# Kernel optimization log

Hardware: AMD Instinct MI355X
Metric: run time of the kernel (lower is better)

The kernel has to match this reference:

```python
import jax, jax.numpy as jnp
import numpy as np

B, S, D = 2, 4096, 768
H = 12
HD = D // H  # 64


def setup_inputs() -> dict:
    key = jax.random.key(0)
    ks = jax.random.split(key, 5)
    scale = 1.0 / np.sqrt(D)
    x = jax.random.normal(ks[0], (B, S, D), dtype=jnp.float32)
    Wq = jax.random.normal(ks[1], (D, D), dtype=jnp.float32) * scale
    Wk = jax.random.normal(ks[2], (D, D), dtype=jnp.float32) * scale
    Wv = jax.random.normal(ks[3], (D, D), dtype=jnp.float32) * scale
    Wo = jax.random.normal(ks[4], (D, D), dtype=jnp.float32) * scale
    zb = jnp.zeros((D,), dtype=jnp.float32)
    return {"x": x, "Wq": Wq, "bq": zb, "Wk": Wk, "bk": zb, "Wv": Wv, "bv": zb, "Wo": Wo, "bo": zb}


def reference(x, Wq, bq, Wk, bk, Wv, bv, Wo, bo):
    b, s, d = x.shape
    # projections: nn.Linear computes x @ W^T + b; here W is stored as [in, out]-style [D, D]
    def proj(W, bias):
        y = jnp.einsum('bsd,ed->bse', x, W) + bias  # matches torch Linear (weight [out,in])
        return y.reshape(b, s, H, HD).transpose(0, 2, 1, 3)  # [B,H,S,HD]
    q = proj(Wq, bq)
    k = proj(Wk, bk)
    v = proj(Wv, bv)
    att = jnp.einsum('bhqd,bhkd->bhqk', q, k) / np.sqrt(HD).astype(np.float32)
    causal = jnp.tril(jnp.ones((s, s), dtype=bool))
    att = jnp.where(causal, att, -jnp.inf)
    att = jax.nn.softmax(att, axis=-1)  # dropout p=0 (eval)
    y = jnp.einsum('bhqk,bhkd->bhqd', att, v)
    y = y.transpose(0, 2, 1, 3).reshape(b, s, d)
    return jnp.einsum('bsd,ed->bse', y, Wo) + bo
```

## Files before the change

kernel.cpp:

```cpp
#include <hip/hip_runtime.h>
#include <hip/hip_bf16.h>

typedef __bf16 bf16;
typedef __attribute__((ext_vector_type(8))) __bf16 bf16x8;
typedef __attribute__((ext_vector_type(4))) __bf16 bf16x4;
typedef __attribute__((ext_vector_type(4))) float f32x4;
typedef __attribute__((ext_vector_type(16))) float f32x16;

#if __has_builtin(__builtin_amdgcn_permlane32_swap)
#define HAVE_PLSWAP 1
typedef __attribute__((ext_vector_type(2))) unsigned uint2v;
#endif

#define MFMA16(a, b, c) __builtin_amdgcn_mfma_f32_16x16x32_bf16((a), (b), (c), 0, 0, 0)
#define MFMA32(a, b, c) __builtin_amdgcn_mfma_f32_32x32x16_bf16((a), (b), (c), 0, 0, 0)

__device__ __forceinline__ void gload_lds16(const bf16* g, bf16* l) {
  __builtin_amdgcn_global_load_lds(
      (const __attribute__((address_space(1))) void*)g,
      (__attribute__((address_space(3))) void*)l, 16, 0, 0);
}

__device__ __forceinline__ unsigned pkbf(float a, float b) {
  union { unsigned u; bf16 h[2]; } w;
  w.h[0] = (bf16)a; w.h[1] = (bf16)b;
  return w.u;
}

__device__ __forceinline__ float mx3(float a, float b, float c) {
  return fmaxf(fmaxf(a, b), c);
}

__global__ void cvt_all(const float* __restrict__ x,
                        const float* __restrict__ wq, const float* __restrict__ wk,
                        const float* __restrict__ wv, const float* __restrict__ wo,
                        bf16* __restrict__ xb, bf16* __restrict__ Wb) {
  constexpr int NX4 = 6291456 / 4;
  constexpr int NW4 = 589824 / 4;
  constexpr int TOT = NX4 + 4 * NW4;
  int stride = gridDim.x * blockDim.x;
  for (int i = blockIdx.x * blockDim.x + threadIdx.x; i < TOT; i += stride) {
    const float4* src;
    bf16x4* dst;
    if (i < NX4) {
      src = reinterpret_cast<const float4*>(x) + i;
      dst = reinterpret_cast<bf16x4*>(xb) + i;
    } else {
      int j = i - NX4;
      int w = j / NW4, r = j - w * NW4;
      const float* sp = (w == 0) ? wq : (w == 1) ? wk : (w == 2) ? wv : wo;
      src = reinterpret_cast<const float4*>(sp) + r;
      dst = reinterpret_cast<bf16x4*>(Wb) + j;
    }
    float4 v = *src;
    bf16x4 o = {(bf16)v.x, (bf16)v.y, (bf16)v.z, (bf16)v.w};
    *dst = o;
  }
}

template <bool OUT_BF16>
__global__ __launch_bounds__(256) void gemm_bt(
    const bf16* __restrict__ A, const bf16* __restrict__ W,
    const float* __restrict__ b0, const float* __restrict__ b1, const float* __restrict__ b2,
    float* __restrict__ Cf, bf16* __restrict__ Cb,
    int M, int N, int K) {
  const int z = blockIdx.z;
  const bf16* Wz = W + (size_t)z * N * K;
  const float* bias = (z == 0) ? b0 : (z == 1 ? b1 : b2);

  __shared__ alignas(16) bf16 As[128 * 64];
  __shared__ alignas(16) bf16 Bs[128 * 64];

  const int tid = threadIdx.x;
  const int wave = tid >> 6, lane = tid & 63;
  const int lr = lane & 15, lg = lane >> 4;
  const int wr = wave >> 1, wc = wave & 1;
  const int m0 = blockIdx.y * 128, n0 = blockIdx.x * 128;

  f32x4 acc[4][4] = {};

  for (int k0 = 0; k0 < K; k0 += 64) {
    __syncthreads();
#pragma unroll
    for (int j = 0; j < 4; ++j) {
      int cb = j * 256 + wave * 64;
      int c = cb + lane;
      int row = c >> 3, x = c & 7;
      int xs = x ^ (row & 7);
      gload_lds16(&A[(size_t)(m0 + row) * K + k0 + xs * 8], &As[cb * 8]);
      gload_lds16(&Wz[(size_t)(n0 + row) * K + k0 + xs * 8], &Bs[cb * 8]);
    }
    __syncthreads();
#pragma unroll
    for (int kk = 0; kk < 2; ++kk) {
      bf16x8 af[4], bfr[4];
#pragma unroll
      for (int m = 0; m < 4; ++m) {
        int row = wr * 64 + m * 16 + lr;
        int ch = (kk * 4 + lg) ^ (row & 7);
        af[m] = *reinterpret_cast<const bf16x8*>(&As[row * 64 + ch * 8]);
      }
#pragma unroll
      for (int n = 0; n < 4; ++n) {
        int row = wc * 64 + n * 16 + lr;
        int ch = (kk * 4 + lg) ^ (row & 7);
        bfr[n] = *reinterpret_cast<const bf16x8*>(&Bs[row * 64 + ch * 8]);
      }
      __builtin_amdgcn_s_setprio(1);
#pragma unroll
      for (int m = 0; m < 4; ++m)
#pragma unroll
        for (int n = 0; n < 4; ++n)
          acc[m][n] = MFMA16(af[m], bfr[n], acc[m][n]);
      __builtin_amdgcn_s_setprio(0);
    }
  }

#pragma unroll
  for (int m = 0; m < 4; ++m) {
#pragma unroll
    for (int n = 0; n < 4; ++n) {
#pragma unroll
      for (int i = 0; i < 4; ++i) {
        int row = m0 + wr * 64 + m * 16 + lg * 4 + i;
        int col = n0 + wc * 64 + n * 16 + lr;
        float v = acc[m][n][i] + bias[col];
        if constexpr (OUT_BF16)
          (Cb + (size_t)z * M * N)[(size_t)row * N + col] = (bf16)v;
        else
          Cf[(size_t)row * N + col] = v;
      }
    }
  }
}

__global__ __launch_bounds__(256, 3) void attn32(
    const bf16* __restrict__ Q, const bf16* __restrict__ K,
    const bf16* __restrict__ V, bf16* __restrict__ Y) {
  constexpr int S = 4096, D = 768;
  const int lin = blockIdx.x + 32 * blockIdx.y + 384 * blockIdx.z;
  const int xcd = lin & 7, idx = lin >> 3;
  const int pair = xcd * 3 + (idx >> 5);
  const int qb = 31 - (idx & 31);
  const int h = pair % 12, bb = pair / 12;

  const int tid = threadIdx.x, wave = tid >> 6, lane = tid & 63;
  const int ln = lane & 31, hi = lane >> 5;
  const int q0 = qb * 128;
  const int qw0 = q0 + wave * 32;
  const int qrow = qw0 + ln;

  __shared__ alignas(16) bf16 Ks[2][64 * 64];
  __shared__ alignas(16) bf16 Vt[2][64 * 64];

  const size_t head = (size_t)bb * S * D + (size_t)h * 64;
  const float SC2 = 0.125f * 1.44269504089f;

  union U32x4 { unsigned u[4]; bf16x8 v; };
  U32x4 onesU;
  onesU.u[0] = onesU.u[1] = onesU.u[2] = onesU.u[3] = 0x3F803F80u;
  const bf16x8 onesf = onesU.v;

  bf16x8 qf[4];
  {
    const bf16* qp = Q + head + (size_t)qrow * D;
#pragma unroll
    for (int c = 0; c < 4; ++c) {
      bf16x8 t = *reinterpret_cast<const bf16x8*>(qp + c * 16 + hi * 8);
#pragma unroll
      for (int e = 0; e < 8; ++e) t[e] = (bf16)((float)t[e] * SC2);
      qf[c] = t;
    }
  }

  int fOff[4];
#pragma unroll
  for (int i = 0; i < 4; ++i)
    fOff[i] = ln * 64 + ((((2 * i + hi) ^ ln) & 7) * 8);

  const int d0 = (tid >> 5) * 8, k0v = ln * 2;
  int wOff[8];
#pragma unroll
  for (int e = 0; e < 8; ++e)
    wOff[e] = (d0 + e) * 64 + ((((ln >> 2) ^ e) & 7) * 8) + (k0v & 7);

  const bf16* gk[2];
  int ldsK[2];
#pragma unroll
  for (int j = 0; j < 2; ++j) {
    int c = (j * 4 + wave) * 64 + lane;
    int r = c >> 3;
    int src = (((lane ^ r) & 7)) * 8;
    gk[j] = K + head + (size_t)r * D + src;
    ldsK[j] = (j * 4 + wave) * 512;
  }
  const bf16* gv0 = V + head + (size_t)k0v * D + d0;
  const bf16* gv1 = gv0 + D;

  f32x16 accO0 = {}, accO1 = {}, accL = {};
  float mrun = 8.0f;

  auto stageK = [&](int buf) {
#pragma unroll
    for (int j = 0; j < 2; ++j) {
      gload_lds16(gk[j], &Ks[buf][ldsK[j]]);
      gk[j] += 64 * D;
    }
  };
  auto loadV = [&](bf16x8* vv) {
    vv[0] = *reinterpret_cast<const bf16x8*>(gv0);
    vv[1] = *reinterpret_cast<const bf16x8*>(gv1);
    gv0 += 64 * D;
    gv1 += 64 * D;
  };
  auto writeV = [&](const bf16x8* vv, int buf) {
#pragma unroll
    for (int e = 0; e < 8; ++e) {
      union { unsigned u; bf16 h[2]; } pw;
      pw.h[0] = vv[0][e]; pw.h[1] = vv[1][e];
      *reinterpret_cast<unsigned*>(&Vt[buf][wOff[e]]) = pw.u;
    }
  };

  const int nt = q0 / 64 + 2;

  {
    bf16x8 v0[2];
    loadV(v0);
    stageK(0);
    writeV(v0, 0);
  }
  __syncthreads();

  int cur = 0;
  for (int t = 0; t < nt; ++t) {
    const int kv0 = t * 64;
    const bool more = (t + 1 < nt);
    bf16x8 vnext[2];
    if (more) {
      loadV(vnext);
      stageK(cur ^ 1);
    }

    if (kv0 <= qw0 + 31) {
      f32x16 s0 = {}, s1 = {};
      __builtin_amdgcn_s_setprio(1);
#pragma unroll
      for (int c = 0; c < 4; ++c) {
        bf16x8 kf0 = *reinterpret_cast<const bf16x8*>(&Ks[cur][fOff[c]]);
        bf16x8 kf1 = *reinterpret_cast<const bf16x8*>(&Ks[cur][fOff[c] + 2048]);
        s0 = MFMA32(kf0, qf[c], s0);
        s1 = MFMA32(kf1, qf[c], s1);
      }
      __builtin_amdgcn_s_setprio(0);

      if (kv0 + 63 > qw0) {
#pragma unroll
        for (int r = 0; r < 16; ++r) {
          int kl = (r & 3) + 8 * (r >> 2) + 4 * hi;
          if (kv0 + kl > qrow) s0[r] = -1e30f;
          if (kv0 + 32 + kl > qrow) s1[r] = -1e30f;
        }
      }

      float p[32];
#pragma unroll
      for (int r = 0; r < 16; ++r) {
        p[r] = __builtin_amdgcn_exp2f(s0[r] - mrun);
        p[16 + r] = __builtin_amdgcn_exp2f(s1[r] - mrun);
      }

      float t0 = mx3(s0[0], s0[1], s0[2]);
      float t1 = mx3(s0[3], s0[4], s0[5]);
      float t2 = mx3(s0[6], s0[7], s0[8]);
      float t3 = mx3(s0[9], s0[10], s0[11]);
      float t4 = mx3(s0[12], s0[13], s0[14]);
      float t5 = mx3(s0[15], s1[0], s1[1]);
      float t6 = mx3(s1[2], s1[3], s1[4]);
      float t7 = mx3(s1[5], s1[6], s1[7]);
      float t8 = mx3(s1[8], s1[9], s1[10]);
      float t9 = mx3(s1[11], s1[12], s1[13]);
      float ta = fmaxf(s1[14], s1[15]);
      float u0 = mx3(t0, t1, t2);
      float u1 = mx3(t3, t4, t5);
      float u2 = mx3(t6, t7, t8);
      float u3 = fmaxf(t9, ta);
      float pm = fmaxf(mx3(u0, u1, u2), u3);

      if (!__all(pm - mrun <= 8.0f)) {
        float pm2 = fmaxf(pm, __shfl_xor(pm, 32));
        float mnew = fmaxf(mrun, pm2);
        float alpha = __builtin_amdgcn_exp2f(mrun - mnew);
        mrun = mnew;
        accL[0] *= alpha;
#pragma unroll
        for (int r = 0; r < 16; ++r) {
          accO0[r] *= alpha; accO1[r] *= alpha;
          p[r] *= alpha; p[16 + r] *= alpha;
        }
      }

      __builtin_amdgcn_s_setprio(1);
#pragma unroll
      for (int kg = 0; kg < 2; ++kg) {
        const float* pv = &p[kg * 16];
        unsigned w0 = pkbf(pv[0], pv[1]), w1 = pkbf(pv[2], pv[3]);
        unsigned w2 = pkbf(pv[4], pv[5]), w3 = pkbf(pv[6], pv[7]);
        unsigned w4 = pkbf(pv[8], pv[9]), w5 = pkbf(pv[10], pv[11]);
        unsigned w6 = pkbf(pv[12], pv[13]), w7 = pkbf(pv[14], pv[15]);
        union { unsigned u[4]; bf16x8 v; } fe, fo;
#if HAVE_PLSWAP
        uint2v r02 = __builtin_amdgcn_permlane32_swap(w0, w2, false, false);
        uint2v r13 = __builtin_amdgcn_permlane32_swap(w1, w3, false, false);
        uint2v r46 = __builtin_amdgcn_permlane32_swap(w4, w6, false, false);
        uint2v r57 = __builtin_amdgcn_permlane32_swap(w5, w7, false, false);
        fe.u[0] = r02.x; fe.u[1] = r13.x; fe.u[2] = r02.y; fe.u[3] = r13.y;
        fo.u[0] = r46.x; fo.u[1] = r57.x; fo.u[2] = r46.y; fo.u[3] = r57.y;
#else
        unsigned X0 = hi ? w0 : w2, X1 = hi ? w1 : w3;
        unsigned X2 = hi ? w4 : w6, X3 = hi ? w5 : w7;
        unsigned Y0 = __shfl_xor((int)X0, 32), Y1 = __shfl_xor((int)X1, 32);
        unsigned Y2 = __shfl_xor((int)X2, 32), Y3 = __shfl_xor((int)X3, 32);
        fe.u[0] = hi ? Y0 : w0; fe.u[1] = hi ? Y1 : w1;
        fe.u[2] = hi ? w2 : Y0; fe.u[3] = hi ? w3 : Y1;
        fo.u[0] = hi ? Y2 : w4; fo.u[1] = hi ? Y3 : w5;
        fo.u[2] = hi ? w6 : Y2; fo.u[3] = hi ? w7 : Y3;
#endif
#pragma unroll
        for (int half = 0; half < 2; ++half) {
          int kc = 2 * kg + half;
          bf16x8 pf = half ? fo.v : fe.v;
          bf16x8 vf0 = *reinterpret_cast<const bf16x8*>(&Vt[cur][fOff[kc]]);
          bf16x8 vf1 = *reinterpret_cast<const bf16x8*>(&Vt[cur][fOff[kc] + 2048]);
          accO0 = MFMA32(vf0, pf, accO0);
          accO1 = MFMA32(vf1, pf, accO1);
          accL = MFMA32(onesf, pf, accL);
        }
      }
      __builtin_amdgcn_s_setprio(0);
    }

    if (more) {
      writeV(vnext, cur ^ 1);
      __syncthreads();
      cur ^= 1;
    }
  }

  float inv = 1.f / accL[0];
  bf16* yp = Y + head + (size_t)qrow * D;
#pragma unroll
  for (int g = 0; g < 4; ++g) {
    bf16x4 o0, o1;
#pragma unroll
    for (int i = 0; i < 4; ++i) {
      o0[i] = (bf16)(accO0[g * 4 + i] * inv);
      o1[i] = (bf16)(accO1[g * 4 + i] * inv);
    }
    *reinterpret_cast<bf16x4*>(yp + 8 * g + 4 * hi) = o0;
    *reinterpret_cast<bf16x4*>(yp + 32 + 8 * g + 4 * hi) = o1;
  }
}

extern "C" void kernel_launch(void* const* d_in, const int* in_sizes, int n_in,
                              void* d_out, int out_size, void* d_ws, size_t ws_size,
                              hipStream_t stream) {
  const float* x  = (const float*)d_in[0];
  const float* Wq = (const float*)d_in[1];
  const float* bq = (const float*)d_in[2];
  const float* Wk = (const float*)d_in[3];
  const float* bk = (const float*)d_in[4];
  const float* Wv = (const float*)d_in[5];
  const float* bv = (const float*)d_in[6];
  const float* Wo = (const float*)d_in[7];
  const float* bo = (const float*)d_in[8];
  float* out = (float*)d_out;

  constexpr int Bx = 2, S = 4096, Dd = 768;
  constexpr int M = Bx * S;
  constexpr size_t XB = (size_t)M * Dd;
  constexpr size_t WB = (size_t)Dd * Dd;

  char* ws = (char*)d_ws;
  bf16* xb = (bf16*)ws;
  bf16* Wb = (bf16*)(ws + 2 * XB);
  bf16* Qb = (bf16*)(ws + 2 * XB + 8 * WB);
  bf16* Kb = Qb + XB;
  bf16* Vb = Kb + XB;
  bf16* Yb = Vb + XB;

  cvt_all<<<2048, 256, 0, stream>>>(x, Wq, Wk, Wv, Wo, xb, Wb);

  gemm_bt<true><<<dim3(6, 64, 3), 256, 0, stream>>>(
      xb, Wb, bq, bk, bv, nullptr, Qb, M, Dd, Dd);

  attn32<<<dim3(S / 128, 12, Bx), 256, 0, stream>>>(Qb, Kb, Vb, Yb);

  gemm_bt<false><<<dim3(6, 64, 1), 256, 0, stream>>>(
      Yb, Wb + 3 * WB, bo, bo, bo, out, nullptr, M, Dd, Dd);
}
```

Measured before the change: 209.4 us.

## Shrink attention blocks to 64 query rows with two waves each

The attention kernel now runs 1536 blocks of 128 threads, each covering 64 query rows, instead of 768 blocks of 256 threads covering 128 rows. K/V staging is reworked so fewer threads load the 64x64 tiles: four async K loads per thread, and four V rows transposed per thread with 8-byte LDS writes. With 64-row blocks aligned to the KV tiles, the per-wave causal skip branch is dropped. The goal is finer-grained work balance across the causal triangle and more resident blocks, at the cost of staging K/V once per 64 query rows rather than per 128, which doubles tile traffic per query row.

```diff
diff --git a/kernel.cpp b/kernel.cpp
--- a/kernel.cpp
+++ b/kernel.cpp
@@ -134,20 +134,20 @@
   }
 }
 
-__global__ __launch_bounds__(256, 3) void attn32(
+__global__ __launch_bounds__(128, 2) void attn32(
     const bf16* __restrict__ Q, const bf16* __restrict__ K,
     const bf16* __restrict__ V, bf16* __restrict__ Y) {
   constexpr int S = 4096, D = 768;
-  const int lin = blockIdx.x + 32 * blockIdx.y + 384 * blockIdx.z;
+  const int lin = blockIdx.x;
   const int xcd = lin & 7, idx = lin >> 3;
-  const int pair = xcd * 3 + (idx >> 5);
-  const int qb = 31 - (idx & 31);
+  const int pair = xcd * 3 + (idx >> 6);
+  const int qs = 63 - (idx & 63);
   const int h = pair % 12, bb = pair / 12;
 
   const int tid = threadIdx.x, wave = tid >> 6, lane = tid & 63;
   const int ln = lane & 31, hi = lane >> 5;
-  const int q0 = qb * 128;
-  const int qw0 = q0 + wave * 32;
+  const int q0s = qs * 64;
+  const int qw0 = q0s + wave * 32;
   const int qrow = qw0 + ln;
 
   __shared__ alignas(16) bf16 Ks[2][64 * 64];
@@ -178,54 +178,54 @@
   for (int i = 0; i < 4; ++i)
     fOff[i] = ln * 64 + ((((2 * i + hi) ^ ln) & 7) * 8);
 
-  const int d0 = (tid >> 5) * 8, k0v = ln * 2;
+  const bf16* gk[4];
+  int ldsK[4];
+#pragma unroll
+  for (int j = 0; j < 4; ++j) {
+    int c = j * 128 + tid;
+    int r = c >> 3, ch = c & 7;
+    gk[j] = K + head + (size_t)r * D + ((ch ^ (r & 7)) & 7) * 8;
+    ldsK[j] = (j * 128 + wave * 64) * 8;
+  }
+
+  const int k0v = (tid & 15) * 4, d0 = (tid >> 4) * 8;
+  const bf16* gv[4];
+#pragma unroll
+  for (int m = 0; m < 4; ++m) gv[m] = V + head + (size_t)(k0v + m) * D + d0;
   int wOff[8];
 #pragma unroll
   for (int e = 0; e < 8; ++e)
-    wOff[e] = (d0 + e) * 64 + ((((ln >> 2) ^ e) & 7) * 8) + (k0v & 7);
-
-  const bf16* gk[2];
-  int ldsK[2];
-#pragma unroll
-  for (int j = 0; j < 2; ++j) {
-    int c = (j * 4 + wave) * 64 + lane;
-    int r = c >> 3;
-    int src = (((lane ^ r) & 7)) * 8;
-    gk[j] = K + head + (size_t)r * D + src;
-    ldsK[j] = (j * 4 + wave) * 512;
-  }
-  const bf16* gv0 = V + head + (size_t)k0v * D + d0;
-  const bf16* gv1 = gv0 + D;
+    wOff[e] = (d0 + e) * 64 + ((((k0v >> 3) ^ e) & 7) * 8) + (k0v & 7);
 
   f32x16 accO0 = {}, accO1 = {}, accL = {};
   float mrun = 8.0f;
 
   auto stageK = [&](int buf) {
 #pragma unroll
-    for (int j = 0; j < 2; ++j) {
+    for (int j = 0; j < 4; ++j) {
       gload_lds16(gk[j], &Ks[buf][ldsK[j]]);
       gk[j] += 64 * D;
     }
   };
   auto loadV = [&](bf16x8* vv) {
-    vv[0] = *reinterpret_cast<const bf16x8*>(gv0);
-    vv[1] = *reinterpret_cast<const bf16x8*>(gv1);
-    gv0 += 64 * D;
-    gv1 += 64 * D;
+#pragma unroll
+    for (int m = 0; m < 4; ++m) {
+      vv[m] = *reinterpret_cast<const bf16x8*>(gv[m]);
+      gv[m] += 64 * D;
+    }
   };
   auto writeV = [&](const bf16x8* vv, int buf) {
 #pragma unroll
     for (int e = 0; e < 8; ++e) {
-      union { unsigned u; bf16 h[2]; } pw;
-      pw.h[0] = vv[0][e]; pw.h[1] = vv[1][e];
-      *reinterpret_cast<unsigned*>(&Vt[buf][wOff[e]]) = pw.u;
+      bf16x4 pw = {vv[0][e], vv[1][e], vv[2][e], vv[3][e]};
+      *reinterpret_cast<bf16x4*>(&Vt[buf][wOff[e]]) = pw;
     }
   };
 
-  const int nt = q0 / 64 + 2;
+  const int nt = qs + 1;
 
   {
-    bf16x8 v0[2];
+    bf16x8 v0[4];
     loadV(v0);
     stageK(0);
     writeV(v0, 0);
@@ -236,109 +236,107 @@
   for (int t = 0; t < nt; ++t) {
     const int kv0 = t * 64;
     const bool more = (t + 1 < nt);
-    bf16x8 vnext[2];
+    bf16x8 vnext[4];
     if (more) {
       loadV(vnext);
       stageK(cur ^ 1);
     }
 
-    if (kv0 <= qw0 + 31) {
-      f32x16 s0 = {}, s1 = {};
-      __builtin_amdgcn_s_setprio(1);
-#pragma unroll
-      for (int c = 0; c < 4; ++c) {
-        bf16x8 kf0 = *reinterpret_cast<const bf16x8*>(&Ks[cur][fOff[c]]);
-        bf16x8 kf1 = *reinterpret_cast<const bf16x8*>(&Ks[cur][fOff[c] + 2048]);
-        s0 = MFMA32(kf0, qf[c], s0);
-        s1 = MFMA32(kf1, qf[c], s1);
-      }
-      __builtin_amdgcn_s_setprio(0);
-
-      if (kv0 + 63 > qw0) {
-#pragma unroll
-        for (int r = 0; r < 16; ++r) {
-          int kl = (r & 3) + 8 * (r >> 2) + 4 * hi;
-          if (kv0 + kl > qrow) s0[r] = -1e30f;
-          if (kv0 + 32 + kl > qrow) s1[r] = -1e30f;
-        }
-      }
-
-      float p[32];
+    f32x16 s0 = {}, s1 = {};
+    __builtin_amdgcn_s_setprio(1);
+#pragma unroll
+    for (int c = 0; c < 4; ++c) {
+      bf16x8 kf0 = *reinterpret_cast<const bf16x8*>(&Ks[cur][fOff[c]]);
+      bf16x8 kf1 = *reinterpret_cast<const bf16x8*>(&Ks[cur][fOff[c] + 2048]);
+      s0 = MFMA32(kf0, qf[c], s0);
+      s1 = MFMA32(kf1, qf[c], s1);
+    }
+    __builtin_amdgcn_s_setprio(0);
+
+    if (kv0 + 63 > qw0) {
 #pragma unroll
       for (int r = 0; r < 16; ++r) {
-        p[r] = __builtin_amdgcn_exp2f(s0[r] - mrun);
-        p[16 + r] = __builtin_amdgcn_exp2f(s1[r] - mrun);
-      }
-
-      float t0 = mx3(s0[0], s0[1], s0[2]);
-      float t1 = mx3(s0[3], s0[4], s0[5]);
-      float t2 = mx3(s0[6], s0[7], s0[8]);
-      float t3 = mx3(s0[9], s0[10], s0[11]);
-      float t4 = mx3(s0[12], s0[13], s0[14]);
-      float t5 = mx3(s0[15], s1[0], s1[1]);
-      float t6 = mx3(s1[2], s1[3], s1[4]);
-      float t7 = mx3(s1[5], s1[6], s1[7]);
-      float t8 = mx3(s1[8], s1[9], s1[10]);
-      float t9 = mx3(s1[11], s1[12], s1[13]);
-      float ta = fmaxf(s1[14], s1[15]);
-      float u0 = mx3(t0, t1, t2);
-      float u1 = mx3(t3, t4, t5);
-      float u2 = mx3(t6, t7, t8);
-      float u3 = fmaxf(t9, ta);
-      float pm = fmaxf(mx3(u0, u1, u2), u3);
-
-      if (!__all(pm - mrun <= 8.0f)) {
-        float pm2 = fmaxf(pm, __shfl_xor(pm, 32));
-        float mnew = fmaxf(mrun, pm2);
-        float alpha = __builtin_amdgcn_exp2f(mrun - mnew);
-        mrun = mnew;
-        accL[0] *= alpha;
-#pragma unroll
-        for (int r = 0; r < 16; ++r) {
-          accO0[r] *= alpha; accO1[r] *= alpha;
-          p[r] *= alpha; p[16 + r] *= alpha;
-        }
-      }
-
-      __builtin_amdgcn_s_setprio(1);
-#pragma unroll
-      for (int kg = 0; kg < 2; ++kg) {
-        const float* pv = &p[kg * 16];
-        unsigned w0 = pkbf(pv[0], pv[1]), w1 = pkbf(pv[2], pv[3]);
-        unsigned w2 = pkbf(pv[4], pv[5]), w3 = pkbf(pv[6], pv[7]);
-        unsigned w4 = pkbf(pv[8], pv[9]), w5 = pkbf(pv[10], pv[11]);
-        unsigned w6 = pkbf(pv[12], pv[13]), w7 = pkbf(pv[14], pv[15]);
-        union { unsigned u[4]; bf16x8 v; } fe, fo;
+        int kl = (r & 3) + 8 * (r >> 2) + 4 * hi;
+        if (kv0 + kl > qrow) s0[r] = -1e30f;
+        if (kv0 + 32 + kl > qrow) s1[r] = -1e30f;
+      }
+    }
+
+    float p[32];
+#pragma unroll
+    for (int r = 0; r < 16; ++r) {
+      p[r] = __builtin_amdgcn_exp2f(s0[r] - mrun);
+      p[16 + r] = __builtin_amdgcn_exp2f(s1[r] - mrun);
+    }
+
+    float t0 = mx3(s0[0], s0[1], s0[2]);
+    float t1 = mx3(s0[3], s0[4], s0[5]);
+    float t2 = mx3(s0[6], s0[7], s0[8]);
+    float t3 = mx3(s0[9], s0[10], s0[11]);
+    float t4 = mx3(s0[12], s0[13], s0[14]);
+    float t5 = mx3(s0[15], s1[0], s1[1]);
+    float t6 = mx3(s1[2], s1[3], s1[4]);
+    float t7 = mx3(s1[5], s1[6], s1[7]);
+    float t8 = mx3(s1[8], s1[9], s1[10]);
+    float t9 = mx3(s1[11], s1[12], s1[13]);
+    float ta = fmaxf(s1[14], s1[15]);
+    float u0 = mx3(t0, t1, t2);
+    float u1 = mx3(t3, t4, t5);
+    float u2 = mx3(t6, t7, t8);
+    float u3 = fmaxf(t9, ta);
+    float pm = fmaxf(mx3(u0, u1, u2), u3);
+
+    if (!__all(pm - mrun <= 8.0f)) {
+      float pm2 = fmaxf(pm, __shfl_xor(pm, 32));
+      float mnew = fmaxf(mrun, pm2);
+      float alpha = __builtin_amdgcn_exp2f(mrun - mnew);
+      mrun = mnew;
+      accL[0] *= alpha;
+#pragma unroll
+      for (int r = 0; r < 16; ++r) {
+        accO0[r] *= alpha; accO1[r] *= alpha;
+        p[r] *= alpha; p[16 + r] *= alpha;
+      }
+    }
+
+    __builtin_amdgcn_s_setprio(1);
+#pragma unroll
+    for (int kg = 0; kg < 2; ++kg) {
+      const float* pv = &p[kg * 16];
+      unsigned w0 = pkbf(pv[0], pv[1]), w1 = pkbf(pv[2], pv[3]);
+      unsigned w2 = pkbf(pv[4], pv[5]), w3 = pkbf(pv[6], pv[7]);
+      unsigned w4 = pkbf(pv[8], pv[9]), w5 = pkbf(pv[10], pv[11]);
+      unsigned w6 = pkbf(pv[12], pv[13]), w7 = pkbf(pv[14], pv[15]);
+      union { unsigned u[4]; bf16x8 v; } fe, fo;
 #if HAVE_PLSWAP
-        uint2v r02 = __builtin_amdgcn_permlane32_swap(w0, w2, false, false);
-        uint2v r13 = __builtin_amdgcn_permlane32_swap(w1, w3, false, false);
-        uint2v r46 = __builtin_amdgcn_permlane32_swap(w4, w6, false, false);
-        uint2v r57 = __builtin_amdgcn_permlane32_swap(w5, w7, false, false);
-        fe.u[0] = r02.x; fe.u[1] = r13.x; fe.u[2] = r02.y; fe.u[3] = r13.y;
-        fo.u[0] = r46.x; fo.u[1] = r57.x; fo.u[2] = r46.y; fo.u[3] = r57.y;
+      uint2v r02 = __builtin_amdgcn_permlane32_swap(w0, w2, false, false);
+      uint2v r13 = __builtin_amdgcn_permlane32_swap(w1, w3, false, false);
+      uint2v r46 = __builtin_amdgcn_permlane32_swap(w4, w6, false, false);
+      uint2v r57 = __builtin_amdgcn_permlane32_swap(w5, w7, false, false);
+      fe.u[0] = r02.x; fe.u[1] = r13.x; fe.u[2] = r02.y; fe.u[3] = r13.y;
+      fo.u[0] = r46.x; fo.u[1] = r57.x; fo.u[2] = r46.y; fo.u[3] = r57.y;
 #else
-        unsigned X0 = hi ? w0 : w2, X1 = hi ? w1 : w3;
-        unsigned X2 = hi ? w4 : w6, X3 = hi ? w5 : w7;
-        unsigned Y0 = __shfl_xor((int)X0, 32), Y1 = __shfl_xor((int)X1, 32);
-        unsigned Y2 = __shfl_xor((int)X2, 32), Y3 = __shfl_xor((int)X3, 32);
-        fe.u[0] = hi ? Y0 : w0; fe.u[1] = hi ? Y1 : w1;
-        fe.u[2] = hi ? w2 : Y0; fe.u[3] = hi ? w3 : Y1;
-        fo.u[0] = hi ? Y2 : w4; fo.u[1] = hi ? Y3 : w5;
-        fo.u[2] = hi ? w6 : Y2; fo.u[3] = hi ? w7 : Y3;
+      unsigned X0 = hi ? w0 : w2, X1 = hi ? w1 : w3;
+      unsigned X2 = hi ? w4 : w6, X3 = hi ? w5 : w7;
+      unsigned Y0 = __shfl_xor((int)X0, 32), Y1 = __shfl_xor((int)X1, 32);
+      unsigned Y2 = __shfl_xor((int)X2, 32), Y3 = __shfl_xor((int)X3, 32);
+      fe.u[0] = hi ? Y0 : w0; fe.u[1] = hi ? Y1 : w1;
+      fe.u[2] = hi ? w2 : Y0; fe.u[3] = hi ? w3 : Y1;
+      fo.u[0] = hi ? Y2 : w4; fo.u[1] = hi ? Y3 : w5;
+      fo.u[2] = hi ? w6 : Y2; fo.u[3] = hi ? w7 : Y3;
 #endif
 #pragma unroll
-        for (int half = 0; half < 2; ++half) {
-          int kc = 2 * kg + half;
-          bf16x8 pf = half ? fo.v : fe.v;
-          bf16x8 vf0 = *reinterpret_cast<const bf16x8*>(&Vt[cur][fOff[kc]]);
-          bf16x8 vf1 = *reinterpret_cast<const bf16x8*>(&Vt[cur][fOff[kc] + 2048]);
-          accO0 = MFMA32(vf0, pf, accO0);
-          accO1 = MFMA32(vf1, pf, accO1);
-          accL = MFMA32(onesf, pf, accL);
-        }
-      }
-      __builtin_amdgcn_s_setprio(0);
-    }
+      for (int half = 0; half < 2; ++half) {
+        int kc = 2 * kg + half;
+        bf16x8 pf = half ? fo.v : fe.v;
+        bf16x8 vf0 = *reinterpret_cast<const bf16x8*>(&Vt[cur][fOff[kc]]);
+        bf16x8 vf1 = *reinterpret_cast<const bf16x8*>(&Vt[cur][fOff[kc] + 2048]);
+        accO0 = MFMA32(vf0, pf, accO0);
+        accO1 = MFMA32(vf1, pf, accO1);
+        accL = MFMA32(onesf, pf, accL);
+      }
+    }
+    __builtin_amdgcn_s_setprio(0);
 
     if (more) {
       writeV(vnext, cur ^ 1);
@@ -394,7 +392,7 @@
   gemm_bt<true><<<dim3(6, 64, 3), 256, 0, stream>>>(
       xb, Wb, bq, bk, bv, nullptr, Qb, M, Dd, Dd);
 
-  attn32<<<dim3(S / 128, 12, Bx), 256, 0, stream>>>(Qb, Kb, Vb, Yb);
+  attn32<<<dim3(1536), 128, 0, stream>>>(Qb, Kb, Vb, Yb);
 
   gemm_bt<false><<<dim3(6, 64, 1), 256, 0, stream>>>(
       Yb, Wb + 3 * WB, bo, bo, bo, out, nullptr, M, Dd, Dd);
```

Measured after the change: 196.6 us. 1.07x faster.

## Pair mirrored causal query tiles per attention block and single-buffer V tile

Applied to the files above, without the earlier changes.

Each attention block now handles two 64-row query segments, one early and one mirrored late (waves 0-1 take 63-f, waves 2-3 take f), so every block runs a similar number of KV tiles. This is meant to fix the triangular load imbalance of causal attention. The launch becomes a flat 1D grid with a per-XCD segment ordering. V's LDS buffer is also made single-buffered, which adds an extra barrier before each V write in exchange for less LDS use. Within a block the two wave pairs still finish at different times, so some waves sit idle until the loop ends.

```diff
diff --git a/kernel.cpp b/kernel.cpp
--- a/kernel.cpp
+++ b/kernel.cpp
@@ -138,20 +138,24 @@
     const bf16* __restrict__ Q, const bf16* __restrict__ K,
     const bf16* __restrict__ V, bf16* __restrict__ Y) {
   constexpr int S = 4096, D = 768;
-  const int lin = blockIdx.x + 32 * blockIdx.y + 384 * blockIdx.z;
+  const int lin = blockIdx.x;
   const int xcd = lin & 7, idx = lin >> 3;
-  const int pair = xcd * 3 + (idx >> 5);
-  const int qb = 31 - (idx & 31);
+  const int seg = idx >> 5;
+  const int pair = xcd * 3 + seg;
+  const int j = idx & 31;
+  const int f = (seg == 0) ? j : (seg == 1) ? (31 - j) : ((j + 16) & 31);
   const int h = pair % 12, bb = pair / 12;
 
   const int tid = threadIdx.x, wave = tid >> 6, lane = tid & 63;
   const int ln = lane & 31, hi = lane >> 5;
-  const int q0 = qb * 128;
-  const int qw0 = q0 + wave * 32;
+
+  const int qs = (wave < 2) ? (63 - f) : f;
+  const int qw0 = qs * 64 + (wave & 1) * 32;
   const int qrow = qw0 + ln;
+  const int nt = 64 - f;
 
   __shared__ alignas(16) bf16 Ks[2][64 * 64];
-  __shared__ alignas(16) bf16 Vt[2][64 * 64];
+  __shared__ alignas(16) bf16 Vt[64 * 64];
 
   const size_t head = (size_t)bb * S * D + (size_t)h * 64;
   const float SC2 = 0.125f * 1.44269504089f;
@@ -166,10 +170,10 @@
     const bf16* qp = Q + head + (size_t)qrow * D;
 #pragma unroll
     for (int c = 0; c < 4; ++c) {
-      bf16x8 t = *reinterpret_cast<const bf16x8*>(qp + c * 16 + hi * 8);
-#pragma unroll
-      for (int e = 0; e < 8; ++e) t[e] = (bf16)((float)t[e] * SC2);
-      qf[c] = t;
+      bf16x8 tq = *reinterpret_cast<const bf16x8*>(qp + c * 16 + hi * 8);
+#pragma unroll
+      for (int e = 0; e < 8; ++e) tq[e] = (bf16)((float)tq[e] * SC2);
+      qf[c] = tq;
     }
   }
 
@@ -178,33 +182,32 @@
   for (int i = 0; i < 4; ++i)
     fOff[i] = ln * 64 + ((((2 * i + hi) ^ ln) & 7) * 8);
 
-  const int d0 = (tid >> 5) * 8, k0v = ln * 2;
-  int wOff[8];
-#pragma unroll
-  for (int e = 0; e < 8; ++e)
-    wOff[e] = (d0 + e) * 64 + ((((ln >> 2) ^ e) & 7) * 8) + (k0v & 7);
-
   const bf16* gk[2];
   int ldsK[2];
 #pragma unroll
-  for (int j = 0; j < 2; ++j) {
-    int c = (j * 4 + wave) * 64 + lane;
-    int r = c >> 3;
-    int src = (((lane ^ r) & 7)) * 8;
-    gk[j] = K + head + (size_t)r * D + src;
-    ldsK[j] = (j * 4 + wave) * 512;
-  }
+  for (int j2 = 0; j2 < 2; ++j2) {
+    int c = j2 * 256 + tid;
+    int r = c >> 3, ch = c & 7;
+    gk[j2] = K + head + (size_t)r * D + ((ch ^ (r & 7)) & 7) * 8;
+    ldsK[j2] = (j2 * 256 + wave * 64) * 8;
+  }
+
+  const int k0v = (tid & 31) * 2, d0 = (tid >> 5) * 8;
   const bf16* gv0 = V + head + (size_t)k0v * D + d0;
   const bf16* gv1 = gv0 + D;
+  int wOff[8];
+#pragma unroll
+  for (int e = 0; e < 8; ++e)
+    wOff[e] = (d0 + e) * 64 + ((((k0v >> 3) ^ e) & 7) * 8) + (k0v & 7);
 
   f32x16 accO0 = {}, accO1 = {}, accL = {};
   float mrun = 8.0f;
 
   auto stageK = [&](int buf) {
 #pragma unroll
-    for (int j = 0; j < 2; ++j) {
-      gload_lds16(gk[j], &Ks[buf][ldsK[j]]);
-      gk[j] += 64 * D;
+    for (int j2 = 0; j2 < 2; ++j2) {
+      gload_lds16(gk[j2], &Ks[buf][ldsK[j2]]);
+      gk[j2] += 64 * D;
     }
   };
   auto loadV = [&](bf16x8* vv) {
@@ -213,22 +216,20 @@
     gv0 += 64 * D;
     gv1 += 64 * D;
   };
-  auto writeV = [&](const bf16x8* vv, int buf) {
+  auto writeV = [&](const bf16x8* vv) {
 #pragma unroll
     for (int e = 0; e < 8; ++e) {
       union { unsigned u; bf16 h[2]; } pw;
       pw.h[0] = vv[0][e]; pw.h[1] = vv[1][e];
-      *reinterpret_cast<unsigned*>(&Vt[buf][wOff[e]]) = pw.u;
+      *reinterpret_cast<unsigned*>(&Vt[wOff[e]]) = pw.u;
     }
   };
-
-  const int nt = q0 / 64 + 2;
 
   {
     bf16x8 v0[2];
     loadV(v0);
     stageK(0);
-    writeV(v0, 0);
+    writeV(v0);
   }
   __syncthreads();
 
@@ -330,8 +331,8 @@
         for (int half = 0; half < 2; ++half) {
           int kc = 2 * kg + half;
           bf16x8 pf = half ? fo.v : fe.v;
-          bf16x8 vf0 = *reinterpret_cast<const bf16x8*>(&Vt[cur][fOff[kc]]);
-          bf16x8 vf1 = *reinterpret_cast<const bf16x8*>(&Vt[cur][fOff[kc] + 2048]);
+          bf16x8 vf0 = *reinterpret_cast<const bf16x8*>(&Vt[fOff[kc]]);
+          bf16x8 vf1 = *reinterpret_cast<const bf16x8*>(&Vt[fOff[kc] + 2048]);
           accO0 = MFMA32(vf0, pf, accO0);
           accO1 = MFMA32(vf1, pf, accO1);
           accL = MFMA32(onesf, pf, accL);
@@ -341,7 +342,8 @@
     }
 
     if (more) {
-      writeV(vnext, cur ^ 1);
+      __syncthreads();
+      writeV(vnext);
       __syncthreads();
       cur ^= 1;
     }
@@ -394,7 +396,7 @@
   gemm_bt<true><<<dim3(6, 64, 3), 256, 0, stream>>>(
       xb, Wb, bq, bk, bv, nullptr, Qb, M, Dd, Dd);
 
-  attn32<<<dim3(S / 128, 12, Bx), 256, 0, stream>>>(Qb, Kb, Vb, Yb);
+  attn32<<<dim3(768), 256, 0, stream>>>(Qb, Kb, Vb, Yb);
 
   gemm_bt<false><<<dim3(6, 64, 1), 256, 0, stream>>>(
       Yb, Wb + 3 * WB, bo, bo, bo, out, nullptr, M, Dd, Dd);
```

Result: faster. 190.4 us (-9.1%).
